# Kernel optimization log

Measured on AMD Instinct MI355X. Metric: run time of the kernel, lower is better.

Reference implementation:

```python
import jax, jax.numpy as jnp
import numpy as np

EMB = 768
HEADS = 12
HEAD_DIM = EMB // HEADS
LAMBDA_INIT = 0.5
LN_EPS = 1e-5


def _rope_tables(seq_len, head_dim):
    # theta_j = 10000^{-2j/d}, j = 0..d/2-1 (standard RoPE)
    j = jnp.arange(head_dim // 2, dtype=jnp.float32)
    theta = jnp.power(10000.0, -2.0 * j / head_dim)            # [d/2]
    ang = jnp.arange(seq_len, dtype=jnp.float32)[:, None] * theta[None, :]  # [S, d/2]
    return jnp.cos(ang), jnp.sin(ang)


def _apply_rope(x, cos, sin):
    # x: [B, H, S, D]; cos/sin: [S, D/2]; rotate consecutive pairs (2j, 2j+1)
    x1 = x[..., 0::2]
    x2 = x[..., 1::2]
    c = cos[None, None, :, :]
    s = sin[None, None, :, :]
    r1 = x1 * c - x2 * s
    r2 = x1 * s + x2 * c
    return jnp.stack([r1, r2], axis=-1).reshape(x.shape)


def setup_inputs() -> dict:
    key = jax.random.key(0)
    ks = jax.random.split(key, 10)
    B, S, E = 2, 2048, EMB
    sd = 1.0 / np.sqrt(E)
    return {
        "x": jax.random.normal(ks[0], (B, S, E), jnp.float32),
        "Wq": jax.random.normal(ks[1], (E, 2 * E), jnp.float32) * sd,
        "bq": jnp.zeros((2 * E,), jnp.float32),
        "Wk": jax.random.normal(ks[2], (E, 2 * E), jnp.float32) * sd,
        "bk": jnp.zeros((2 * E,), jnp.float32),
        "Wv": jax.random.normal(ks[3], (E, E), jnp.float32) * sd,
        "bv": jnp.zeros((E,), jnp.float32),
        "Wo": jax.random.normal(ks[4], (E, E), jnp.float32) * sd,
        "bo": jnp.zeros((E,), jnp.float32),
        "q_scale": jnp.ones((1, 1, 2 * E), jnp.float32),
        "k_scale": jnp.ones((1, 1, 2 * E), jnp.float32),
        "v_scale": jnp.ones((1, 1, E), jnp.float32),
        "o_scale": jnp.ones((1, 1, E), jnp.float32),
        "lambda_param": jnp.asarray(0.0, jnp.float32),
    }


def reference(x, Wq, bq, Wk, bk, Wv, bv, Wo, bo,
              q_scale, k_scale, v_scale, o_scale, lambda_param):
    B, S, E = x.shape
    H, D = HEADS, HEAD_DIM

    Q = (x @ Wq + bq) * q_scale          # [B, S, 2E]
    K = (x @ Wk + bk) * k_scale          # [B, S, 2E]
    V = (x @ Wv + bv) * v_scale          # [B, S, E]

    Q1, Q2 = jnp.split(Q, 2, axis=-1)
    K1, K2 = jnp.split(K, 2, axis=-1)

    def to_heads(t):  # [B, S, E] -> [B, H, S, D]
        return t.reshape(B, S, H, D).transpose(0, 2, 1, 3)

    Q1, Q2, K1, K2, Vh = map(to_heads, (Q1, Q2, K1, K2, V))

    cos, sin = _rope_tables(S, D)
    Q1, Q2 = _apply_rope(Q1, cos, sin), _apply_rope(Q2, cos, sin)
    K1, K2 = _apply_rope(K1, cos, sin), _apply_rope(K2, cos, sin)

    scale = 1.0 / jnp.sqrt(jnp.asarray(D, jnp.float32))
    p1 = jax.nn.softmax(jnp.einsum("bhqd,bhkd->bhqk", Q1, K1) * scale, axis=-1)
    p2 = jax.nn.softmax(jnp.einsum("bhqd,bhkd->bhqk", Q2, K2) * scale, axis=-1)

    lam = jax.nn.sigmoid(lambda_param)
    ctx = jnp.einsum("bhqk,bhkd->bhqd", p1 - lam * p2, Vh)  # [B, H, S, D]

    # layer_norm over head_dim, no affine params
    mu = jnp.mean(ctx, axis=-1, keepdims=True)
    var = jnp.mean(jnp.square(ctx - mu), axis=-1, keepdims=True)
    ctx = (ctx - mu) * jax.lax.rsqrt(var + LN_EPS)

    ctx = ctx * (1.0 - LAMBDA_INIT)
    ctx = ctx.transpose(0, 2, 1, 3).reshape(B, S, E)
    return (ctx @ Wo + bo) * o_scale
```

## Files before the change

kernel.cpp:

```cpp
#include <hip/hip_runtime.h>
#include <hip/hip_bf16.h>

#define BB 2
#define SS 2048
#define EE 768
#define HH 12
#define DD 64
#define MM (BB*SS)

typedef __bf16 bf16_t;
typedef __bf16 bf16x8 __attribute__((ext_vector_type(8)));
typedef __bf16 bf16x4 __attribute__((ext_vector_type(4)));
typedef float  f32x4  __attribute__((ext_vector_type(4)));

static __device__ __forceinline__ f32x4 mfma16(bf16x8 a, bf16x8 b, f32x4 c) {
    return __builtin_amdgcn_mfma_f32_16x16x32_bf16(a, b, c, 0, 0, 0);
}

static __device__ __forceinline__ void gload_lds16(const bf16_t* g, bf16_t* l) {
    __builtin_amdgcn_global_load_lds(
        (const __attribute__((address_space(1))) void*)g,
        (__attribute__((address_space(3))) void*)l,
        16, 0, 0);
}

__global__ __launch_bounds__(256)
void prep_kernel(const float* __restrict__ x,
                 const float* __restrict__ Wq, const float* __restrict__ Wk,
                 const float* __restrict__ Wv, const float* __restrict__ Wo,
                 bf16_t* __restrict__ xb,
                 bf16_t* __restrict__ WqT, bf16_t* __restrict__ WkT,
                 bf16_t* __restrict__ WvT, bf16_t* __restrict__ WoT,
                 float* __restrict__ ctab, float* __restrict__ stab)
{
    __shared__ float tile[32][33];
    const int bx = blockIdx.x, tid = threadIdx.x;

    if (bx < 1536) {
        int i = (bx * 256 + tid) * 8;
        float4 a = *reinterpret_cast<const float4*>(x + i);
        float4 b = *reinterpret_cast<const float4*>(x + i + 4);
        bf16x8 v;
        v[0] = (bf16_t)a.x; v[1] = (bf16_t)a.y; v[2] = (bf16_t)a.z; v[3] = (bf16_t)a.w;
        v[4] = (bf16_t)b.x; v[5] = (bf16_t)b.y; v[6] = (bf16_t)b.z; v[7] = (bf16_t)b.w;
        *reinterpret_cast<bf16x8*>(xb + i) = v;
        return;
    }
    if (bx < 1792) {
        int t = (bx - 1536) * 256 + tid;
        int s = t >> 5, j = t & 31;
        float theta = exp2f(-(float)j * (13.287712379549449f / 32.0f));
        float ang = (float)s * theta;
        float sn, cs;
        sincosf(ang, &sn, &cs);
        ctab[t] = cs;
        stab[t] = sn;
        return;
    }
    int idx = bx - 1792;
    const float* W; bf16_t* WT; int N;
    if (idx < 1152)      { W = Wq; WT = WqT; N = 1536; }
    else if (idx < 2304) { W = Wk; WT = WkT; N = 1536; idx -= 1152; }
    else if (idx < 2880) { W = Wv; WT = WvT; N = 768;  idx -= 2304; }
    else                 { W = Wo; WT = WoT; N = 768;  idx -= 2880; }
    const int ntiles = N >> 5;
    const int n0 = (idx % ntiles) * 32, k0 = (idx / ntiles) * 32;
    const int tx = tid & 31, ty = tid >> 5;
    #pragma unroll
    for (int r = 0; r < 32; r += 8)
        tile[ty + r][tx] = W[(size_t)(k0 + ty + r) * N + n0 + tx];
    __syncthreads();
    #pragma unroll
    for (int r = 0; r < 32; r += 8)
        WT[(size_t)(n0 + ty + r) * 768 + k0 + tx] = (bf16_t)tile[tx][ty + r];
}

__global__ __launch_bounds__(256)
void gemm_qkv_kernel(const bf16_t* __restrict__ xb,
                     const bf16_t* __restrict__ WqT, const bf16_t* __restrict__ WkT,
                     const bf16_t* __restrict__ WvT,
                     const float* __restrict__ bq, const float* __restrict__ bk,
                     const float* __restrict__ bv,
                     const float* __restrict__ qs, const float* __restrict__ ks,
                     const float* __restrict__ vs,
                     const float* __restrict__ ctab, const float* __restrict__ stab,
                     bf16_t* __restrict__ Qr, bf16_t* __restrict__ Kr, bf16_t* __restrict__ Vt)
{
    __shared__ __align__(16) bf16_t sm[17408];
    bf16_t* As = sm;
    bf16_t* Bs = sm + 8192;
    const int tid = threadIdx.x;
    const int w = tid >> 6, lane = tid & 63, q15 = lane & 15, g = lane >> 4;
    const int m0 = blockIdx.x * 128;
    const int nt = blockIdx.y;

    const bf16_t* Wsrc; const float* bias; const float* scale;
    int nloc0, mode; bf16_t* dstQK = nullptr; float qmul = 1.0f;
    if (nt < 12)      { Wsrc = WqT; bias = bq; scale = qs; nloc0 = nt * 128;        mode = 0; dstQK = Qr;
                        qmul = 0.125f * 1.4426950408889634f; }
    else if (nt < 24) { Wsrc = WkT; bias = bk; scale = ks; nloc0 = (nt - 12) * 128; mode = 0; dstQK = Kr; }
    else              { Wsrc = WvT; bias = bv; scale = vs; nloc0 = (nt - 24) * 128; mode = 1; }

    f32x4 acc[4][4];
    #pragma unroll
    for (int i = 0; i < 4; ++i)
        #pragma unroll
        for (int j = 0; j < 4; ++j)
            acc[i][j] = f32x4{0.f, 0.f, 0.f, 0.f};

    const bf16_t* gA[4]; const bf16_t* gB[4]; bf16_t* lA[4]; bf16_t* lB[4];
    #pragma unroll
    for (int c = 0; c < 4; ++c) {
        int t16 = c * 256 + tid;
        int row = t16 >> 3;
        int sc16 = (t16 & 7) ^ (row & 7);
        gA[c] = &xb[(size_t)(m0 + row) * 768 + sc16 * 8];
        gB[c] = &Wsrc[(size_t)(nloc0 + row) * 768 + sc16 * 8];
        lA[c] = &As[(c * 256 + w * 64) * 8];
        lB[c] = &Bs[(c * 256 + w * 64) * 8];
    }

    const int ar0 = (w >> 1) * 64, bc0 = (w & 1) * 64;
    const int xr = q15 & 7;

    for (int k0 = 0; k0 < 768; k0 += 64) {
        if (k0) __syncthreads();
        #pragma unroll
        for (int c = 0; c < 4; ++c) {
            gload_lds16(gA[c] + k0, lA[c]);
            gload_lds16(gB[c] + k0, lB[c]);
        }
        __syncthreads();
        #pragma unroll
        for (int st = 0; st < 2; ++st) {
            const int cA = ((4 * st + g) ^ xr) * 8;
            bf16x8 af[4], bfr[4];
            #pragma unroll
            for (int i = 0; i < 4; ++i)
                af[i] = *reinterpret_cast<const bf16x8*>(&As[(ar0 + i * 16 + q15) * 64 + cA]);
            #pragma unroll
            for (int j = 0; j < 4; ++j)
                bfr[j] = *reinterpret_cast<const bf16x8*>(&Bs[(bc0 + j * 16 + q15) * 64 + cA]);
            #pragma unroll
            for (int i = 0; i < 4; ++i)
                #pragma unroll
                for (int j = 0; j < 4; ++j)
                    acc[i][j] = mfma16(af[i], bfr[j], acc[i][j]);
        }
    }

    const int mbase = m0 + (w >> 1) * 64;
    const int nbase = nloc0 + (w & 1) * 64;

    if (mode == 1) {
        __syncthreads();
        #pragma unroll
        for (int j = 0; j < 4; ++j) {
            const int nl = (w & 1) * 64 + j * 16 + q15;
            const int n = nloc0 + nl;
            const float bi = bias[n], sc = scale[n];
            #pragma unroll
            for (int i = 0; i < 4; ++i) {
                const int ml = (w >> 1) * 64 + i * 16 + g * 4;
                #pragma unroll
                for (int r = 0; r < 4; ++r)
                    sm[nl * 136 + ml + r] = (bf16_t)((acc[i][j][r] + bi) * sc);
            }
        }
        __syncthreads();
        const int nl = tid >> 1, mh = (tid & 1) * 64;
        const int n = nloc0 + nl, h = n >> 6, d = n & 63;
        const int b = m0 >> 11, sbase = (m0 & 2047) + mh;
        bf16_t* dst = Vt + ((size_t)(b * HH + h) * DD + d) * SS + sbase;
        #pragma unroll
        for (int c = 0; c < 8; ++c)
            *reinterpret_cast<bf16x8*>(dst + c * 8) =
                *reinterpret_cast<const bf16x8*>(&sm[nl * 136 + mh + c * 8]);
        return;
    }

    #pragma unroll
    for (int j = 0; j < 4; ++j) {
        const int n = nbase + j * 16 + q15;
        const float bi = bias[n];
        const float sc = scale[n] * qmul;
        const int br = (n >= 768) ? 1 : 0;
        const int n2 = n - br * 768;
        const int h = n2 >> 6, d = n2 & 63, jj = d >> 1;
        #pragma unroll
        for (int i = 0; i < 4; ++i)
            #pragma unroll
            for (int r = 0; r < 4; ++r) {
                int m = mbase + i * 16 + g * 4 + r;
                int b = m >> 11, s = m & 2047;
                float v = (acc[i][j][r] + bi) * sc;
                float p = __shfl_xor(v, 1);
                float cs = ctab[s * 32 + jj], sn = stab[s * 32 + jj];
                float outv = (d & 1) ? (p * sn + v * cs) : (v * cs - p * sn);
                dstQK[(((size_t)(b * 2 + br) * HH + h) * SS + s) * DD + d] = (bf16_t)outv;
            }
    }
}

__global__ __launch_bounds__(256)
void attn_kernel(const bf16_t* __restrict__ Qr, const bf16_t* __restrict__ Kr,
                 const bf16_t* __restrict__ Vt, const float* __restrict__ lambda_param,
                 bf16_t* __restrict__ ctx)
{
    __shared__ __align__(16) char smem[27648];
    bf16_t (*K1s)[72] = (bf16_t (*)[72])(smem);
    bf16_t (*K2s)[72] = (bf16_t (*)[72])(smem + 9216);
    bf16_t (*Vs)[72]  = (bf16_t (*)[72])(smem + 18432);
    float  (*Cb)[68]  = (float  (*)[68])(smem);

    const int idlin = blockIdx.x;
    const int work = ((idlin & 7) * 96) + (idlin >> 3);
    const int bh = work >> 5, b = bh / HH, h = bh % HH;
    const int s0 = (work & 31) * 64;
    const int tid = threadIdx.x, w = tid >> 6, lane = tid & 63, q15 = lane & 15, g = lane >> 4;
    const int br = w >> 1, half = w & 1;

    const bf16_t* Qp = Qr + (((size_t)(b * 2 + br) * HH + h) * SS + (s0 + half * 32 + q15)) * DD;
    bf16x8 qf[2][2];
    #pragma unroll
    for (int j = 0; j < 2; ++j)
        #pragma unroll
        for (int st = 0; st < 2; ++st)
            qf[j][st] = *reinterpret_cast<const bf16x8*>(Qp + (size_t)j * 16 * DD + st * 32 + g * 8);

    const bf16_t* K1base = Kr + ((size_t)(b * 2 + 0) * HH + h) * SS * DD;
    const bf16_t* K2base = Kr + ((size_t)(b * 2 + 1) * HH + h) * SS * DD;
    const bf16_t* Vbase  = Vt + ((size_t)b * HH + h) * DD * SS;

    f32x4 lacc[2];
    f32x4 O[2][4];
    #pragma unroll
    for (int j = 0; j < 2; ++j) {
        lacc[j] = f32x4{0.f, 0.f, 0.f, 0.f};
        #pragma unroll
        for (int df = 0; df < 4; ++df)
            O[j][df] = f32x4{0.f, 0.f, 0.f, 0.f};
    }
    bf16x8 onesv;
    #pragma unroll
    for (int e = 0; e < 8; ++e) onesv[e] = (bf16_t)1.0f;

    const int srow = tid >> 3, scol = (tid & 7) * 8;
    const int u0 = (scol & 32) + ((scol & 15) >> 2) * 8 + ((scol >> 4) & 1) * 4;

    const bf16_t (*Ksb)[72] = br ? K2s : K1s;

    bf16x8 rK1[2], rK2[2], rV[2];
    #pragma unroll
    for (int ii = 0; ii < 2; ++ii) {
        int r2 = srow + ii * 32;
        rK1[ii] = *reinterpret_cast<const bf16x8*>(&K1base[(size_t)r2 * DD + scol]);
        rK2[ii] = *reinterpret_cast<const bf16x8*>(&K2base[(size_t)r2 * DD + scol]);
        rV[ii]  = *reinterpret_cast<const bf16x8*>(&Vbase[(size_t)r2 * SS + scol]);
    }

    for (int kb = 0; kb < SS; kb += 64) {
        if (kb) __syncthreads();
        #pragma unroll
        for (int ii = 0; ii < 2; ++ii) {
            int r2 = srow + ii * 32;
            *reinterpret_cast<bf16x8*>(&K1s[r2][scol]) = rK1[ii];
            *reinterpret_cast<bf16x8*>(&K2s[r2][scol]) = rK2[ii];
            bf16x4 lo = __builtin_shufflevector(rV[ii], rV[ii], 0, 1, 2, 3);
            bf16x4 hi = __builtin_shufflevector(rV[ii], rV[ii], 4, 5, 6, 7);
            *reinterpret_cast<bf16x4*>(&Vs[r2][u0])     = lo;
            *reinterpret_cast<bf16x4*>(&Vs[r2][u0 + 8]) = hi;
        }
        __syncthreads();
        if (kb + 64 < SS) {
            int kn = kb + 64;
            #pragma unroll
            for (int ii = 0; ii < 2; ++ii) {
                int r2 = srow + ii * 32;
                rK1[ii] = *reinterpret_cast<const bf16x8*>(&K1base[(size_t)(kn + r2) * DD + scol]);
                rK2[ii] = *reinterpret_cast<const bf16x8*>(&K2base[(size_t)(kn + r2) * DD + scol]);
                rV[ii]  = *reinterpret_cast<const bf16x8*>(&Vbase[(size_t)r2 * SS + kn + scol]);
            }
        }

        f32x4 sf[2][4];
        #pragma unroll
        for (int rf = 0; rf < 4; ++rf) {
            bf16x8 kf0 = *reinterpret_cast<const bf16x8*>(&Ksb[rf * 16 + q15][g * 8]);
            bf16x8 kf1 = *reinterpret_cast<const bf16x8*>(&Ksb[rf * 16 + q15][32 + g * 8]);
            #pragma unroll
            for (int j = 0; j < 2; ++j) {
                f32x4 a = mfma16(kf0, qf[j][0], f32x4{0.f, 0.f, 0.f, 0.f});
                sf[j][rf] = mfma16(kf1, qf[j][1], a);
            }
        }

        bf16x8 pa[2][2];
        #pragma unroll
        for (int j = 0; j < 2; ++j)
            #pragma unroll
            for (int st = 0; st < 2; ++st)
                #pragma unroll
                for (int e = 0; e < 8; ++e)
                    pa[j][st][e] = (bf16_t)__builtin_amdgcn_exp2f(sf[j][st * 2 + (e >> 2)][e & 3]);

        #pragma unroll
        for (int j = 0; j < 2; ++j) {
            lacc[j] = mfma16(pa[j][0], onesv, lacc[j]);
            lacc[j] = mfma16(pa[j][1], onesv, lacc[j]);
        }

        #pragma unroll
        for (int df = 0; df < 4; ++df) {
            bf16x8 vf0 = *reinterpret_cast<const bf16x8*>(&Vs[df * 16 + q15][g * 8]);
            bf16x8 vf1 = *reinterpret_cast<const bf16x8*>(&Vs[df * 16 + q15][32 + g * 8]);
            #pragma unroll
            for (int j = 0; j < 2; ++j) {
                O[j][df] = mfma16(pa[j][0], vf0, O[j][df]);
                O[j][df] = mfma16(pa[j][1], vf1, O[j][df]);
            }
        }
    }

    __syncthreads();

    if (br == 1) {
        const float lam = 1.0f / (1.0f + __expf(-lambda_param[0]));
        #pragma unroll
        for (int j = 0; j < 2; ++j) {
            #pragma unroll
            for (int r = 0; r < 4; ++r) {
                float inv = lam / lacc[j][r];
                int lq = half * 32 + j * 16 + g * 4 + r;
                #pragma unroll
                for (int df = 0; df < 4; ++df)
                    Cb[lq][df * 16 + q15] = O[j][df][r] * inv;
            }
        }
    }
    __syncthreads();

    if (br == 0) {
        #pragma unroll
        for (int j = 0; j < 2; ++j) {
            #pragma unroll
            for (int r = 0; r < 4; ++r) {
                float inv = 1.0f / lacc[j][r];
                int lq = half * 32 + j * 16 + g * 4 + r;
                float cv[4];
                #pragma unroll
                for (int df = 0; df < 4; ++df)
                    cv[df] = O[j][df][r] * inv - Cb[lq][df * 16 + q15];
                float sum = cv[0] + cv[1] + cv[2] + cv[3];
                sum += __shfl_xor(sum, 1); sum += __shfl_xor(sum, 2);
                sum += __shfl_xor(sum, 4); sum += __shfl_xor(sum, 8);
                float mu = sum * (1.0f / 64.0f);
                float vac = 0.f;
                #pragma unroll
                for (int df = 0; df < 4; ++df) { float dv = cv[df] - mu; vac += dv * dv; }
                vac += __shfl_xor(vac, 1); vac += __shfl_xor(vac, 2);
                vac += __shfl_xor(vac, 4); vac += __shfl_xor(vac, 8);
                float rs = rsqrtf(vac * (1.0f / 64.0f) + 1e-5f);
                int s = s0 + lq;
                size_t rowoff = ((size_t)b * SS + s) * EE + h * DD;
                #pragma unroll
                for (int df = 0; df < 4; ++df)
                    ctx[rowoff + df * 16 + q15] = (bf16_t)((cv[df] - mu) * rs * 0.5f);
            }
        }
    }
}

__global__ __launch_bounds__(256)
void gemm_out_kernel(const bf16_t* __restrict__ ctxb, const bf16_t* __restrict__ WoT,
                     const float* __restrict__ bo, const float* __restrict__ os,
                     float* __restrict__ out)
{
    __shared__ __align__(16) bf16_t As[64 * 64];
    __shared__ __align__(16) bf16_t Bs[128 * 64];
    const int tid = threadIdx.x;
    const int w = tid >> 6, lane = tid & 63, q15 = lane & 15, g = lane >> 4;
    const int m0 = blockIdx.x * 64;
    const int nloc0 = blockIdx.y * 128;

    f32x4 acc[2][4];
    #pragma unroll
    for (int i = 0; i < 2; ++i)
        #pragma unroll
        for (int j = 0; j < 4; ++j)
            acc[i][j] = f32x4{0.f, 0.f, 0.f, 0.f};

    const bf16_t* gA[2]; const bf16_t* gB[4]; bf16_t* lA[2]; bf16_t* lB[4];
    #pragma unroll
    for (int c = 0; c < 2; ++c) {
        int t16 = c * 256 + tid;
        int row = t16 >> 3;
        int sc16 = (t16 & 7) ^ (row & 7);
        gA[c] = &ctxb[(size_t)(m0 + row) * 768 + sc16 * 8];
        lA[c] = &As[(c * 256 + w * 64) * 8];
    }
    #pragma unroll
    for (int c = 0; c < 4; ++c) {
        int t16 = c * 256 + tid;
        int row = t16 >> 3;
        int sc16 = (t16 & 7) ^ (row & 7);
        gB[c] = &WoT[(size_t)(nloc0 + row) * 768 + sc16 * 8];
        lB[c] = &Bs[(c * 256 + w * 64) * 8];
    }

    const int ar0 = (w >> 1) * 32, bc0 = (w & 1) * 64;
    const int xr = q15 & 7;

    for (int k0 = 0; k0 < 768; k0 += 64) {
        if (k0) __syncthreads();
        #pragma unroll
        for (int c = 0; c < 2; ++c) gload_lds16(gA[c] + k0, lA[c]);
        #pragma unroll
        for (int c = 0; c < 4; ++c) gload_lds16(gB[c] + k0, lB[c]);
        __syncthreads();
        #pragma unroll
        for (int st = 0; st < 2; ++st) {
            const int cA = ((4 * st + g) ^ xr) * 8;
            bf16x8 af[2], bfr[4];
            #pragma unroll
            for (int i = 0; i < 2; ++i)
                af[i] = *reinterpret_cast<const bf16x8*>(&As[(ar0 + i * 16 + q15) * 64 + cA]);
            #pragma unroll
            for (int j = 0; j < 4; ++j)
                bfr[j] = *reinterpret_cast<const bf16x8*>(&Bs[(bc0 + j * 16 + q15) * 64 + cA]);
            #pragma unroll
            for (int i = 0; i < 2; ++i)
                #pragma unroll
                for (int j = 0; j < 4; ++j)
                    acc[i][j] = mfma16(af[i], bfr[j], acc[i][j]);
        }
    }

    const int mbase = m0 + (w >> 1) * 32;
    const int nbase = nloc0 + (w & 1) * 64;
    #pragma unroll
    for (int j = 0; j < 4; ++j) {
        const int n = nbase + j * 16 + q15;
        const float bi = bo[n], sc = os[n];
        #pragma unroll
        for (int i = 0; i < 2; ++i)
            #pragma unroll
            for (int r = 0; r < 4; ++r) {
                int m = mbase + i * 16 + g * 4 + r;
                out[(size_t)m * 768 + n] = (acc[i][j][r] + bi) * sc;
            }
    }
}

extern "C" void kernel_launch(void* const* d_in, const int* in_sizes, int n_in,
                              void* d_out, int out_size, void* d_ws, size_t ws_size,
                              hipStream_t stream)
{
    (void)in_sizes; (void)n_in; (void)out_size; (void)ws_size;
    const float* x  = (const float*)d_in[0];
    const float* Wq = (const float*)d_in[1];
    const float* bq = (const float*)d_in[2];
    const float* Wk = (const float*)d_in[3];
    const float* bk = (const float*)d_in[4];
    const float* Wv = (const float*)d_in[5];
    const float* bv = (const float*)d_in[6];
    const float* Wo = (const float*)d_in[7];
    const float* bo = (const float*)d_in[8];
    const float* qs = (const float*)d_in[9];
    const float* ks = (const float*)d_in[10];
    const float* vs = (const float*)d_in[11];
    const float* os = (const float*)d_in[12];
    const float* lp = (const float*)d_in[13];
    float* out = (float*)d_out;

    char* ws = (char*)d_ws;
    bf16_t* xb   = (bf16_t*)(ws);
    bf16_t* WqT  = (bf16_t*)(ws + 6291456);
    bf16_t* WkT  = (bf16_t*)(ws + 8650752);
    bf16_t* WvT  = (bf16_t*)(ws + 11010048);
    bf16_t* WoT  = (bf16_t*)(ws + 12189696);
    bf16_t* Qr   = (bf16_t*)(ws + 13369344);
    bf16_t* Kr   = (bf16_t*)(ws + 25952256);
    bf16_t* Vt   = (bf16_t*)(ws + 38535168);
    bf16_t* ctxb = (bf16_t*)(ws + 44826624);
    float*  ctab = (float*)(ws + 51118080);
    float*  stab = (float*)(ws + 51380224);

    prep_kernel<<<dim3(5248), dim3(256), 0, stream>>>(x, Wq, Wk, Wv, Wo,
                                                      xb, WqT, WkT, WvT, WoT, ctab, stab);
    gemm_qkv_kernel<<<dim3(32, 30), dim3(256), 0, stream>>>(xb, WqT, WkT, WvT,
                                                            bq, bk, bv, qs, ks, vs,
                                                            ctab, stab, Qr, Kr, Vt);
    attn_kernel<<<dim3(768), dim3(256), 0, stream>>>(Qr, Kr, Vt, lp, ctxb);
    gemm_out_kernel<<<dim3(64, 6), dim3(256), 0, stream>>>(ctxb, WoT, bo, os, out);
}
```

Before: 126.1 us.

## Load K and V fragments directly from global memory, dropping LDS staging

```diff
diff --git a/kernel.cpp b/kernel.cpp
--- a/kernel.cpp
+++ b/kernel.cpp
@@ -202,16 +202,12 @@
     }
 }
 
-__global__ __launch_bounds__(256)
+__global__ __launch_bounds__(256, 3)
 void attn_kernel(const bf16_t* __restrict__ Qr, const bf16_t* __restrict__ Kr,
                  const bf16_t* __restrict__ Vt, const float* __restrict__ lambda_param,
                  bf16_t* __restrict__ ctx)
 {
-    __shared__ __align__(16) char smem[27648];
-    bf16_t (*K1s)[72] = (bf16_t (*)[72])(smem);
-    bf16_t (*K2s)[72] = (bf16_t (*)[72])(smem + 9216);
-    bf16_t (*Vs)[72]  = (bf16_t (*)[72])(smem + 18432);
-    float  (*Cb)[68]  = (float  (*)[68])(smem);
+    __shared__ float Cb[64][68];
 
     const int idlin = blockIdx.x;
     const int work = ((idlin & 7) * 96) + (idlin >> 3);
@@ -228,9 +224,8 @@
         for (int st = 0; st < 2; ++st)
             qf[j][st] = *reinterpret_cast<const bf16x8*>(Qp + (size_t)j * 16 * DD + st * 32 + g * 8);
 
-    const bf16_t* K1base = Kr + ((size_t)(b * 2 + 0) * HH + h) * SS * DD;
-    const bf16_t* K2base = Kr + ((size_t)(b * 2 + 1) * HH + h) * SS * DD;
-    const bf16_t* Vbase  = Vt + ((size_t)b * HH + h) * DD * SS;
+    const bf16_t* Kp = Kr + ((size_t)(b * 2 + br) * HH + h) * SS * DD + (size_t)q15 * DD + g * 8;
+    const bf16_t* Vp = Vt + ((size_t)b * HH + h) * DD * SS + (size_t)q15 * SS + g * 4;
 
     f32x4 lacc[2];
     f32x4 O[2][4];
@@ -245,55 +240,35 @@
     #pragma unroll
     for (int e = 0; e < 8; ++e) onesv[e] = (bf16_t)1.0f;
 
-    const int srow = tid >> 3, scol = (tid & 7) * 8;
-    const int u0 = (scol & 32) + ((scol & 15) >> 2) * 8 + ((scol >> 4) & 1) * 4;
-
-    const bf16_t (*Ksb)[72] = br ? K2s : K1s;
-
-    bf16x8 rK1[2], rK2[2], rV[2];
-    #pragma unroll
-    for (int ii = 0; ii < 2; ++ii) {
-        int r2 = srow + ii * 32;
-        rK1[ii] = *reinterpret_cast<const bf16x8*>(&K1base[(size_t)r2 * DD + scol]);
-        rK2[ii] = *reinterpret_cast<const bf16x8*>(&K2base[(size_t)r2 * DD + scol]);
-        rV[ii]  = *reinterpret_cast<const bf16x8*>(&Vbase[(size_t)r2 * SS + scol]);
-    }
-
     for (int kb = 0; kb < SS; kb += 64) {
-        if (kb) __syncthreads();
-        #pragma unroll
-        for (int ii = 0; ii < 2; ++ii) {
-            int r2 = srow + ii * 32;
-            *reinterpret_cast<bf16x8*>(&K1s[r2][scol]) = rK1[ii];
-            *reinterpret_cast<bf16x8*>(&K2s[r2][scol]) = rK2[ii];
-            bf16x4 lo = __builtin_shufflevector(rV[ii], rV[ii], 0, 1, 2, 3);
-            bf16x4 hi = __builtin_shufflevector(rV[ii], rV[ii], 4, 5, 6, 7);
-            *reinterpret_cast<bf16x4*>(&Vs[r2][u0])     = lo;
-            *reinterpret_cast<bf16x4*>(&Vs[r2][u0 + 8]) = hi;
-        }
-        __syncthreads();
-        if (kb + 64 < SS) {
-            int kn = kb + 64;
-            #pragma unroll
-            for (int ii = 0; ii < 2; ++ii) {
-                int r2 = srow + ii * 32;
-                rK1[ii] = *reinterpret_cast<const bf16x8*>(&K1base[(size_t)(kn + r2) * DD + scol]);
-                rK2[ii] = *reinterpret_cast<const bf16x8*>(&K2base[(size_t)(kn + r2) * DD + scol]);
-                rV[ii]  = *reinterpret_cast<const bf16x8*>(&Vbase[(size_t)r2 * SS + kn + scol]);
-            }
-        }
+        const bf16_t* Kt = Kp + (size_t)kb * DD;
+        const bf16_t* Vtp = Vp + kb;
+
+        bf16x8 kf[4][2];
+        #pragma unroll
+        for (int rf = 0; rf < 4; ++rf)
+            #pragma unroll
+            for (int st = 0; st < 2; ++st)
+                kf[rf][st] = *reinterpret_cast<const bf16x8*>(Kt + (size_t)rf * 16 * DD + st * 32);
+
+        bf16x4 vlo[4][2], vhi[4][2];
+        #pragma unroll
+        for (int df = 0; df < 4; ++df)
+            #pragma unroll
+            for (int st = 0; st < 2; ++st) {
+                const bf16_t* vr = Vtp + (size_t)df * 16 * SS + st * 32;
+                vlo[df][st] = *reinterpret_cast<const bf16x4*>(vr);
+                vhi[df][st] = *reinterpret_cast<const bf16x4*>(vr + 16);
+            }
 
         f32x4 sf[2][4];
         #pragma unroll
-        for (int rf = 0; rf < 4; ++rf) {
-            bf16x8 kf0 = *reinterpret_cast<const bf16x8*>(&Ksb[rf * 16 + q15][g * 8]);
-            bf16x8 kf1 = *reinterpret_cast<const bf16x8*>(&Ksb[rf * 16 + q15][32 + g * 8]);
+        for (int rf = 0; rf < 4; ++rf)
             #pragma unroll
             for (int j = 0; j < 2; ++j) {
-                f32x4 a = mfma16(kf0, qf[j][0], f32x4{0.f, 0.f, 0.f, 0.f});
-                sf[j][rf] = mfma16(kf1, qf[j][1], a);
-            }
-        }
+                f32x4 a = mfma16(kf[rf][0], qf[j][0], f32x4{0.f, 0.f, 0.f, 0.f});
+                sf[j][rf] = mfma16(kf[rf][1], qf[j][1], a);
+            }
 
         bf16x8 pa[2][2];
         #pragma unroll
@@ -312,8 +287,8 @@
 
         #pragma unroll
         for (int df = 0; df < 4; ++df) {
-            bf16x8 vf0 = *reinterpret_cast<const bf16x8*>(&Vs[df * 16 + q15][g * 8]);
-            bf16x8 vf1 = *reinterpret_cast<const bf16x8*>(&Vs[df * 16 + q15][32 + g * 8]);
+            bf16x8 vf0 = __builtin_shufflevector(vlo[df][0], vhi[df][0], 0, 1, 2, 3, 4, 5, 6, 7);
+            bf16x8 vf1 = __builtin_shufflevector(vlo[df][1], vhi[df][1], 0, 1, 2, 3, 4, 5, 6, 7);
             #pragma unroll
             for (int j = 0; j < 2; ++j) {
                 O[j][df] = mfma16(pa[j][0], vf0, O[j][df]);
@@ -321,8 +296,6 @@
             }
         }
     }
-
-    __syncthreads();
 
     if (br == 1) {
         const float lam = 1.0f / (1.0f + __expf(-lambda_param[0]));
```

Result: slower. 316.0 us (+150.5%).

## Halve attention query tile to 32 rows and double grid size

Applied to the files above, without the earlier changes.

```diff
diff --git a/kernel.cpp b/kernel.cpp
--- a/kernel.cpp
+++ b/kernel.cpp
@@ -202,7 +202,7 @@
     }
 }
 
-__global__ __launch_bounds__(256)
+__global__ __launch_bounds__(256, 5)
 void attn_kernel(const bf16_t* __restrict__ Qr, const bf16_t* __restrict__ Kr,
                  const bf16_t* __restrict__ Vt, const float* __restrict__ lambda_param,
                  bf16_t* __restrict__ ctx)
@@ -214,33 +214,27 @@
     float  (*Cb)[68]  = (float  (*)[68])(smem);
 
     const int idlin = blockIdx.x;
-    const int work = ((idlin & 7) * 96) + (idlin >> 3);
-    const int bh = work >> 5, b = bh / HH, h = bh % HH;
-    const int s0 = (work & 31) * 64;
+    const int work = ((idlin & 7) * 192) + (idlin >> 3);
+    const int bh = work >> 6, b = bh / HH, h = bh % HH;
+    const int s0 = (work & 63) * 32;
     const int tid = threadIdx.x, w = tid >> 6, lane = tid & 63, q15 = lane & 15, g = lane >> 4;
     const int br = w >> 1, half = w & 1;
 
-    const bf16_t* Qp = Qr + (((size_t)(b * 2 + br) * HH + h) * SS + (s0 + half * 32 + q15)) * DD;
-    bf16x8 qf[2][2];
-    #pragma unroll
-    for (int j = 0; j < 2; ++j)
-        #pragma unroll
-        for (int st = 0; st < 2; ++st)
-            qf[j][st] = *reinterpret_cast<const bf16x8*>(Qp + (size_t)j * 16 * DD + st * 32 + g * 8);
+    const bf16_t* Qp = Qr + (((size_t)(b * 2 + br) * HH + h) * SS + (s0 + half * 16 + q15)) * DD;
+    bf16x8 qf[2];
+    #pragma unroll
+    for (int st = 0; st < 2; ++st)
+        qf[st] = *reinterpret_cast<const bf16x8*>(Qp + st * 32 + g * 8);
 
     const bf16_t* K1base = Kr + ((size_t)(b * 2 + 0) * HH + h) * SS * DD;
     const bf16_t* K2base = Kr + ((size_t)(b * 2 + 1) * HH + h) * SS * DD;
     const bf16_t* Vbase  = Vt + ((size_t)b * HH + h) * DD * SS;
 
-    f32x4 lacc[2];
-    f32x4 O[2][4];
-    #pragma unroll
-    for (int j = 0; j < 2; ++j) {
-        lacc[j] = f32x4{0.f, 0.f, 0.f, 0.f};
-        #pragma unroll
-        for (int df = 0; df < 4; ++df)
-            O[j][df] = f32x4{0.f, 0.f, 0.f, 0.f};
-    }
+    f32x4 lacc = f32x4{0.f, 0.f, 0.f, 0.f};
+    f32x4 O[4];
+    #pragma unroll
+    for (int df = 0; df < 4; ++df)
+        O[df] = f32x4{0.f, 0.f, 0.f, 0.f};
     bf16x8 onesv;
     #pragma unroll
     for (int e = 0; e < 8; ++e) onesv[e] = (bf16_t)1.0f;
@@ -283,42 +277,31 @@
             }
         }
 
-        f32x4 sf[2][4];
+        f32x4 sf[4];
         #pragma unroll
         for (int rf = 0; rf < 4; ++rf) {
             bf16x8 kf0 = *reinterpret_cast<const bf16x8*>(&Ksb[rf * 16 + q15][g * 8]);
             bf16x8 kf1 = *reinterpret_cast<const bf16x8*>(&Ksb[rf * 16 + q15][32 + g * 8]);
-            #pragma unroll
-            for (int j = 0; j < 2; ++j) {
-                f32x4 a = mfma16(kf0, qf[j][0], f32x4{0.f, 0.f, 0.f, 0.f});
-                sf[j][rf] = mfma16(kf1, qf[j][1], a);
-            }
-        }
-
-        bf16x8 pa[2][2];
-        #pragma unroll
-        for (int j = 0; j < 2; ++j)
-            #pragma unroll
-            for (int st = 0; st < 2; ++st)
-                #pragma unroll
-                for (int e = 0; e < 8; ++e)
-                    pa[j][st][e] = (bf16_t)__builtin_amdgcn_exp2f(sf[j][st * 2 + (e >> 2)][e & 3]);
-
-        #pragma unroll
-        for (int j = 0; j < 2; ++j) {
-            lacc[j] = mfma16(pa[j][0], onesv, lacc[j]);
-            lacc[j] = mfma16(pa[j][1], onesv, lacc[j]);
-        }
+            f32x4 a = mfma16(kf0, qf[0], f32x4{0.f, 0.f, 0.f, 0.f});
+            sf[rf] = mfma16(kf1, qf[1], a);
+        }
+
+        bf16x8 pa[2];
+        #pragma unroll
+        for (int st = 0; st < 2; ++st)
+            #pragma unroll
+            for (int e = 0; e < 8; ++e)
+                pa[st][e] = (bf16_t)__builtin_amdgcn_exp2f(sf[st * 2 + (e >> 2)][e & 3]);
+
+        lacc = mfma16(pa[0], onesv, lacc);
+        lacc = mfma16(pa[1], onesv, lacc);
 
         #pragma unroll
         for (int df = 0; df < 4; ++df) {
             bf16x8 vf0 = *reinterpret_cast<const bf16x8*>(&Vs[df * 16 + q15][g * 8]);
             bf16x8 vf1 = *reinterpret_cast<const bf16x8*>(&Vs[df * 16 + q15][32 + g * 8]);
-            #pragma unroll
-            for (int j = 0; j < 2; ++j) {
-                O[j][df] = mfma16(pa[j][0], vf0, O[j][df]);
-                O[j][df] = mfma16(pa[j][1], vf1, O[j][df]);
-            }
+            O[df] = mfma16(pa[0], vf0, O[df]);
+            O[df] = mfma16(pa[1], vf1, O[df]);
         }
     }
 
@@ -327,46 +310,40 @@
     if (br == 1) {
         const float lam = 1.0f / (1.0f + __expf(-lambda_param[0]));
         #pragma unroll
-        for (int j = 0; j < 2; ++j) {
-            #pragma unroll
-            for (int r = 0; r < 4; ++r) {
-                float inv = lam / lacc[j][r];
-                int lq = half * 32 + j * 16 + g * 4 + r;
-                #pragma unroll
-                for (int df = 0; df < 4; ++df)
-                    Cb[lq][df * 16 + q15] = O[j][df][r] * inv;
-            }
+        for (int r = 0; r < 4; ++r) {
+            float inv = lam / lacc[r];
+            int lq = half * 16 + g * 4 + r;
+            #pragma unroll
+            for (int df = 0; df < 4; ++df)
+                Cb[lq][df * 16 + q15] = O[df][r] * inv;
         }
     }
     __syncthreads();
 
     if (br == 0) {
         #pragma unroll
-        for (int j = 0; j < 2; ++j) {
-            #pragma unroll
-            for (int r = 0; r < 4; ++r) {
-                float inv = 1.0f / lacc[j][r];
-                int lq = half * 32 + j * 16 + g * 4 + r;
-                float cv[4];
-                #pragma unroll
-                for (int df = 0; df < 4; ++df)
-                    cv[df] = O[j][df][r] * inv - Cb[lq][df * 16 + q15];
-                float sum = cv[0] + cv[1] + cv[2] + cv[3];
-                sum += __shfl_xor(sum, 1); sum += __shfl_xor(sum, 2);
-                sum += __shfl_xor(sum, 4); sum += __shfl_xor(sum, 8);
-                float mu = sum * (1.0f / 64.0f);
-                float vac = 0.f;
-                #pragma unroll
-                for (int df = 0; df < 4; ++df) { float dv = cv[df] - mu; vac += dv * dv; }
-                vac += __shfl_xor(vac, 1); vac += __shfl_xor(vac, 2);
-                vac += __shfl_xor(vac, 4); vac += __shfl_xor(vac, 8);
-                float rs = rsqrtf(vac * (1.0f / 64.0f) + 1e-5f);
-                int s = s0 + lq;
-                size_t rowoff = ((size_t)b * SS + s) * EE + h * DD;
-                #pragma unroll
-                for (int df = 0; df < 4; ++df)
-                    ctx[rowoff + df * 16 + q15] = (bf16_t)((cv[df] - mu) * rs * 0.5f);
-            }
+        for (int r = 0; r < 4; ++r) {
+            float inv = 1.0f / lacc[r];
+            int lq = half * 16 + g * 4 + r;
+            float cv[4];
+            #pragma unroll
+            for (int df = 0; df < 4; ++df)
+                cv[df] = O[df][r] * inv - Cb[lq][df * 16 + q15];
+            float sum = cv[0] + cv[1] + cv[2] + cv[3];
+            sum += __shfl_xor(sum, 1); sum += __shfl_xor(sum, 2);
+            sum += __shfl_xor(sum, 4); sum += __shfl_xor(sum, 8);
+            float mu = sum * (1.0f / 64.0f);
+            float vac = 0.f;
+            #pragma unroll
+            for (int df = 0; df < 4; ++df) { float dv = cv[df] - mu; vac += dv * dv; }
+            vac += __shfl_xor(vac, 1); vac += __shfl_xor(vac, 2);
+            vac += __shfl_xor(vac, 4); vac += __shfl_xor(vac, 8);
+            float rs = rsqrtf(vac * (1.0f / 64.0f) + 1e-5f);
+            int s = s0 + lq;
+            size_t rowoff = ((size_t)b * SS + s) * EE + h * DD;
+            #pragma unroll
+            for (int df = 0; df < 4; ++df)
+                ctx[rowoff + df * 16 + q15] = (bf16_t)((cv[df] - mu) * rs * 0.5f);
         }
     }
 }
@@ -491,6 +468,6 @@
     gemm_qkv_kernel<<<dim3(32, 30), dim3(256), 0, stream>>>(xb, WqT, WkT, WvT,
                                                             bq, bk, bv, qs, ks, vs,
                                                             ctab, stab, Qr, Kr, Vt);
-    attn_kernel<<<dim3(768), dim3(256), 0, stream>>>(Qr, Kr, Vt, lp, ctxb);
+    attn_kernel<<<dim3(1536), dim3(256), 0, stream>>>(Qr, Kr, Vt, lp, ctxb);
     gemm_out_kernel<<<dim3(64, 6), dim3(256), 0, stream>>>(ctxb, WoT, bo, os, out);
 }
```

New measurement: 146.2 us. 1.16x slower.

## Load K tiles directly to LDS with double-buffered, XOR-swizzled async global_load_lds

Applied to the files above, without the earlier changes.

```diff
diff --git a/kernel.cpp b/kernel.cpp
--- a/kernel.cpp
+++ b/kernel.cpp
@@ -207,11 +207,11 @@
                  const bf16_t* __restrict__ Vt, const float* __restrict__ lambda_param,
                  bf16_t* __restrict__ ctx)
 {
-    __shared__ __align__(16) char smem[27648];
-    bf16_t (*K1s)[72] = (bf16_t (*)[72])(smem);
-    bf16_t (*K2s)[72] = (bf16_t (*)[72])(smem + 9216);
-    bf16_t (*Vs)[72]  = (bf16_t (*)[72])(smem + 18432);
-    float  (*Cb)[68]  = (float  (*)[68])(smem);
+    __shared__ __align__(16) char smem[41984];
+    bf16_t* K1v = (bf16_t*)(smem);
+    bf16_t* K2v = (bf16_t*)(smem + 16384);
+    bf16_t (*Vs)[72] = (bf16_t (*)[72])(smem + 32768);
+    float  (*Cb)[68] = (float  (*)[68])(smem);
 
     const int idlin = blockIdx.x;
     const int work = ((idlin & 7) * 96) + (idlin >> 3);
@@ -248,46 +248,59 @@
     const int srow = tid >> 3, scol = (tid & 7) * 8;
     const int u0 = (scol & 32) + ((scol & 15) >> 2) * 8 + ((scol >> 4) & 1) * 4;
 
-    const bf16_t (*Ksb)[72] = br ? K2s : K1s;
-
-    bf16x8 rK1[2], rK2[2], rV[2];
+    const int krow0 = (lane >> 3);
+    const int kc16  = lane & 7;
+
+    bf16x8 rV[2];
+    #pragma unroll
+    for (int ii = 0; ii < 2; ++ii)
+        rV[ii] = *reinterpret_cast<const bf16x8*>(&Vbase[(size_t)(srow + ii * 32) * SS + scol]);
+
     #pragma unroll
     for (int ii = 0; ii < 2; ++ii) {
-        int r2 = srow + ii * 32;
-        rK1[ii] = *reinterpret_cast<const bf16x8*>(&K1base[(size_t)r2 * DD + scol]);
-        rK2[ii] = *reinterpret_cast<const bf16x8*>(&K2base[(size_t)r2 * DD + scol]);
-        rV[ii]  = *reinterpret_cast<const bf16x8*>(&Vbase[(size_t)r2 * SS + scol]);
+        int row = w * 16 + ii * 8 + krow0;
+        int sc16 = kc16 ^ (row & 7);
+        gload_lds16(&K1base[(size_t)row * DD + sc16 * 8], &K1v[(size_t)(w * 16 + ii * 8) * 64]);
+        gload_lds16(&K2base[(size_t)row * DD + sc16 * 8], &K2v[(size_t)(w * 16 + ii * 8) * 64]);
     }
 
     for (int kb = 0; kb < SS; kb += 64) {
+        const int cur = (kb >> 6) & 1;
         if (kb) __syncthreads();
         #pragma unroll
         for (int ii = 0; ii < 2; ++ii) {
             int r2 = srow + ii * 32;
-            *reinterpret_cast<bf16x8*>(&K1s[r2][scol]) = rK1[ii];
-            *reinterpret_cast<bf16x8*>(&K2s[r2][scol]) = rK2[ii];
             bf16x4 lo = __builtin_shufflevector(rV[ii], rV[ii], 0, 1, 2, 3);
             bf16x4 hi = __builtin_shufflevector(rV[ii], rV[ii], 4, 5, 6, 7);
             *reinterpret_cast<bf16x4*>(&Vs[r2][u0])     = lo;
             *reinterpret_cast<bf16x4*>(&Vs[r2][u0 + 8]) = hi;
         }
         __syncthreads();
+
         if (kb + 64 < SS) {
             int kn = kb + 64;
+            const int nxt = cur ^ 1;
             #pragma unroll
             for (int ii = 0; ii < 2; ++ii) {
-                int r2 = srow + ii * 32;
-                rK1[ii] = *reinterpret_cast<const bf16x8*>(&K1base[(size_t)(kn + r2) * DD + scol]);
-                rK2[ii] = *reinterpret_cast<const bf16x8*>(&K2base[(size_t)(kn + r2) * DD + scol]);
-                rV[ii]  = *reinterpret_cast<const bf16x8*>(&Vbase[(size_t)r2 * SS + kn + scol]);
-            }
-        }
+                int row = w * 16 + ii * 8 + krow0;
+                int sc16 = kc16 ^ (row & 7);
+                gload_lds16(&K1base[(size_t)(kn + row) * DD + sc16 * 8],
+                            &K1v[((size_t)nxt * 64 + w * 16 + ii * 8) * 64]);
+                gload_lds16(&K2base[(size_t)(kn + row) * DD + sc16 * 8],
+                            &K2v[((size_t)nxt * 64 + w * 16 + ii * 8) * 64]);
+                rV[ii] = *reinterpret_cast<const bf16x8*>(
+                    &Vbase[(size_t)(srow + ii * 32) * SS + kn + scol]);
+            }
+        }
+
+        const bf16_t* Kvb = (br ? K2v : K1v) + (size_t)cur * 64 * 64;
 
         f32x4 sf[2][4];
         #pragma unroll
         for (int rf = 0; rf < 4; ++rf) {
-            bf16x8 kf0 = *reinterpret_cast<const bf16x8*>(&Ksb[rf * 16 + q15][g * 8]);
-            bf16x8 kf1 = *reinterpret_cast<const bf16x8*>(&Ksb[rf * 16 + q15][32 + g * 8]);
+            const bf16_t* krow = &Kvb[(size_t)(rf * 16 + q15) * 64];
+            bf16x8 kf0 = *reinterpret_cast<const bf16x8*>(&krow[((g)     ^ (q15 & 7)) * 8]);
+            bf16x8 kf1 = *reinterpret_cast<const bf16x8*>(&krow[((4 + g) ^ (q15 & 7)) * 8]);
             #pragma unroll
             for (int j = 0; j < 2; ++j) {
                 f32x4 a = mfma16(kf0, qf[j][0], f32x4{0.f, 0.f, 0.f, 0.f});
```

New measurement: 124.8 us. About the same (-1.1%).
